# Performance work log

Hardware: AMD Instinct MI355X
Metric: run time of the kernel (lower is better)

## Reference

```python
import jax, jax.numpy as jnp
import numpy as np


def silu(x):
    return x * jax.nn.sigmoid(x)


def conv1x1(x, w, s, b, act):
    # x: [B,Ci,H,W], w: [Co,Ci]; BN folded into per-channel scale s / bias b
    y = jnp.einsum('oi,bihw->bohw', w, x) * s[None, :, None, None] + b[None, :, None, None]
    return silu(y) if act else y


def dwconv3x3(x, w, s, b):
    # depthwise 3x3, groups=C, padding SAME (autopad=1); w: [C,1,3,3]
    y = jax.lax.conv_general_dilated(
        x, w, window_strides=(1, 1), padding=[(1, 1), (1, 1)],
        dimension_numbers=('NCHW', 'OIHW', 'NCHW'),
        feature_group_count=x.shape[1])
    return y * s[None, :, None, None] + b[None, :, None, None]


def attention(x, qkv_w, qkv_s, qkv_b, pe_w, pe_s, pe_b, proj_w, proj_s, proj_b,
              num_heads=4, key_dim=32, head_dim=64):
    B, C, H, W = x.shape
    N = H * W
    scale = key_dim ** -0.5
    qkv = conv1x1(x, qkv_w, qkv_s, qkv_b, act=False)          # [B, C+2*nh*kd, H, W]
    qkv = qkv.reshape(B, num_heads, key_dim * 2 + head_dim, N)
    q = qkv[:, :, :key_dim]                                    # [B,nh,kd,N]
    k = qkv[:, :, key_dim:2 * key_dim]                         # [B,nh,kd,N]
    v = qkv[:, :, 2 * key_dim:]                                # [B,nh,hd,N]
    attn = jnp.einsum('bhdi,bhdj->bhij', q, k) * scale         # [B,nh,N,N]
    attn = jax.nn.softmax(attn, axis=-1)
    out = jnp.einsum('bhdj,bhij->bhdi', v, attn)               # [B,nh,hd,N]
    out = out.reshape(B, C, H, W) + dwconv3x3(v.reshape(B, C, H, W), pe_w, pe_s, pe_b)
    return conv1x1(out, proj_w, proj_s, proj_b, act=False)


def setup_inputs() -> dict:
    key = jax.random.key(0)
    ks = jax.random.split(key, 32)
    B, C1, H, W = 4, 512, 48, 48
    c = C1 // 2  # 256
    h = c + 2 * 32 * 4  # 512
    d = {'x': jax.random.normal(ks[0], (B, C1, H, W), jnp.float32)}
    def w(i, shape):
        return jax.random.normal(ks[i], shape, jnp.float32) * 0.05
    def s(i, n):
        return jax.random.uniform(ks[i], (n,), jnp.float32, 0.5, 1.5)
    def b(i, n):
        return jax.random.normal(ks[i], (n,), jnp.float32) * 0.05
    d['cv1_w'], d['cv1_s'], d['cv1_b'] = w(1, (2 * c, C1)), s(2, 2 * c), b(3, 2 * c)
    d['qkv_w'], d['qkv_s'], d['qkv_b'] = w(4, (h, c)), s(5, h), b(6, h)
    d['pe_w'], d['pe_s'], d['pe_b'] = w(7, (c, 1, 3, 3)), s(8, c), b(9, c)
    d['proj_w'], d['proj_s'], d['proj_b'] = w(10, (c, c)), s(11, c), b(12, c)
    d['ffn1_w'], d['ffn1_s'], d['ffn1_b'] = w(13, (2 * c, c)), s(14, 2 * c), b(15, 2 * c)
    d['ffn2_w'], d['ffn2_s'], d['ffn2_b'] = w(16, (c, 2 * c)), s(17, c), b(18, c)
    d['cv2_w'], d['cv2_s'], d['cv2_b'] = w(19, (C1, 2 * c)), s(20, C1), b(21, C1)
    return d


def reference(x, cv1_w, cv1_s, cv1_b, qkv_w, qkv_s, qkv_b, pe_w, pe_s, pe_b,
              proj_w, proj_s, proj_b, ffn1_w, ffn1_s, ffn1_b, ffn2_w, ffn2_s, ffn2_b,
              cv2_w, cv2_s, cv2_b):
    c = cv1_w.shape[0] // 2  # hidden channels (256)
    ab = conv1x1(x, cv1_w, cv1_s, cv1_b, act=True)
    a, bb = ab[:, :c], ab[:, c:]
    bb = bb + attention(bb, qkv_w, qkv_s, qkv_b, pe_w, pe_s, pe_b,
                        proj_w, proj_s, proj_b)
    f = conv1x1(bb, ffn1_w, ffn1_s, ffn1_b, act=True)
    bb = bb + conv1x1(f, ffn2_w, ffn2_s, ffn2_b, act=False)
    return conv1x1(jnp.concatenate([a, bb], axis=1), cv2_w, cv2_s, cv2_b, act=True)
```

## Files before the change

### kernel.cpp

```cpp
#include <hip/hip_runtime.h>
#include <math.h>

#define N_SP 2304
#define HW 48

typedef unsigned short u16;
typedef short s8v  __attribute__((ext_vector_type(8)));
typedef short s4v  __attribute__((ext_vector_type(4)));
typedef u16   u16x8 __attribute__((ext_vector_type(8)));
typedef float f32x4 __attribute__((ext_vector_type(4)));
typedef unsigned u32x4 __attribute__((ext_vector_type(4)));

__device__ __forceinline__ short f2bf(float x) {
    unsigned u = __float_as_uint(x);
    u += 0x7FFFu + ((u >> 16) & 1u);
    return (short)(u >> 16);
}
__device__ __forceinline__ float bf2f(u16 u) {
    return __uint_as_float((unsigned)u << 16);
}
__device__ __forceinline__ float fexp2(float x) { return __builtin_amdgcn_exp2f(x); }
__device__ __forceinline__ float frcp(float x)  { return __builtin_amdgcn_rcpf(x); }
__device__ __forceinline__ float fsilu(float v) {
    return v * frcp(1.f + fexp2(-1.4426950408889634f * v));
}
__device__ __forceinline__ unsigned cvtpk(float lo, float hi) {
    unsigned r;
    asm("v_cvt_pk_bf16_f32 %0, %1, %2" : "=v"(r) : "v"(lo), "v"(hi));
    return r;
}
__device__ __forceinline__ void gload16(const void* g, void* l) {
    __builtin_amdgcn_global_load_lds(
        (const __attribute__((address_space(1))) void*)g,
        (__attribute__((address_space(3))) void*)l, 16, 0, 0);
}

__global__ __launch_bounds__(256) void cvt_w(
    const float* __restrict__ s0, const float* __restrict__ s1,
    const float* __restrict__ s2, const float* __restrict__ s3,
    const float* __restrict__ s4, const float* __restrict__ s5,
    u16* __restrict__ d0, u16* __restrict__ d1, u16* __restrict__ d2,
    u16* __restrict__ d3, u16* __restrict__ d4, u16* __restrict__ d5)
{
    int id = blockIdx.x * 256 + threadIdx.x;
    const int c0 = 65536, c1 = c0 + 32768, c2 = c1 + 16384,
              c3 = c2 + 32768, c4 = c3 + 32768, c5 = c4 + 65536;
    if (id >= c5) return;
    const float* s; u16* d; int off;
    if      (id < c0) { s = s0; d = d0; off = id; }
    else if (id < c1) { s = s1; d = d1; off = id - c0; }
    else if (id < c2) { s = s2; d = d2; off = id - c1; }
    else if (id < c3) { s = s3; d = d3; off = id - c2; }
    else if (id < c4) { s = s4; d = d4; off = id - c3; }
    else              { s = s5; d = d5; off = id - c4; }
    float4 v = ((const float4*)s)[off];
    s4v p; p[0] = f2bf(v.x); p[1] = f2bf(v.y); p[2] = f2bf(v.z); p[3] = f2bf(v.w);
    ((s4v*)d)[off] = p;
}

__global__ __launch_bounds__(256) void transpose_x(const float* __restrict__ X,
                                                   u16* __restrict__ XT)
{
    __shared__ float tile[64][65];
    const int n0 = blockIdx.x * 64, c0 = blockIdx.y * 64, b = blockIdx.z;
    const float* src = X + (long)b * 512 * N_SP;
    u16* dst = XT + (long)b * N_SP * 512;
    const int t = threadIdx.x;
    #pragma unroll
    for (int it = 0; it < 16; ++it) {
        int id = t + 256 * it;
        int cl = id >> 6, nl = id & 63;
        tile[cl][nl] = src[(long)(c0 + cl) * N_SP + n0 + nl];
    }
    __syncthreads();
    #pragma unroll
    for (int it = 0; it < 16; ++it) {
        int id = t + 256 * it;
        int nl = id >> 6, cl = id & 63;
        dst[(long)(n0 + nl) * 512 + c0 + cl] = f2bf(tile[cl][nl]);
    }
}

template <int BN_, int OMODE>
__global__ __launch_bounds__(256) void mfma_gemm(
    const u16* __restrict__ A1, const u16* __restrict__ A2, int K1,
    int sA1, int sA2, int K,
    const u16* __restrict__ W,
    const float* __restrict__ S, const float* __restrict__ Bi,
    const u16* __restrict__ Res, int sR,
    void* __restrict__ OutP, int sO, int Mtot,
    int act)
{
    constexpr int NFN = BN_ / 32;
    __shared__ u16 Al[2][128][64];
    __shared__ u16 Bl[2][BN_][64];
    const int t  = threadIdx.x;
    const int n0 = blockIdx.x * 128;
    const int o0 = blockIdx.y * BN_;
    const int lane = t & 63, w = t >> 6;
    const int wn = (w & 1) * 64, wo = (w >> 1) * (BN_ / 2);
    const int li = lane & 15, g = lane >> 4;

    const int b_blk = n0 / N_SP;
    const int n_in0 = n0 - b_blk * N_SP;

    f32x4 acc[4][NFN];
    #pragma unroll
    for (int fm = 0; fm < 4; ++fm)
        #pragma unroll
        for (int fn = 0; fn < NFN; ++fn) acc[fm][fn] = f32x4{0.f, 0.f, 0.f, 0.f};

    auto issue = [&](int buf, int k0) {
        #pragma unroll
        for (int q = 0; q < 4; ++q) {
            int c = t + q * 256;
            int row = c >> 3;
            int col = ((c & 7) ^ (row & 7)) * 8;
            int kk = k0 + col;
            const u16* ga = (kk < K1) ? (A1 + (long)(n0 + row) * sA1 + kk)
                                      : (A2 + (long)(n0 + row) * sA2 + (kk - K1));
            gload16(ga, (u16*)Al[buf] + (q * 256 + w * 64) * 8);
        }
        #pragma unroll
        for (int q = 0; q < NFN; ++q) {
            int c = t + q * 256;
            int row = c >> 3;
            int col = ((c & 7) ^ (row & 7)) * 8;
            gload16(W + (long)(o0 + row) * K + k0 + col,
                    (u16*)Bl[buf] + (q * 256 + w * 64) * 8);
        }
    };

    issue(0, 0);
    asm volatile("s_waitcnt vmcnt(0)" ::: "memory");
    __builtin_amdgcn_s_barrier();

    int cur = 0;
    const int NK = K >> 6;
    for (int ks = 0; ks < NK; ++ks) {
        if (ks + 1 < NK) issue(cur ^ 1, (ks + 1) << 6);
        #pragma unroll
        for (int k2 = 0; k2 < 2; ++k2) {
            s8v af[4], bfv[NFN];
            #pragma unroll
            for (int fm = 0; fm < 4; ++fm) {
                int row = wn + fm * 16 + li;
                af[fm] = *(const s8v*)&Al[cur][row][((g + 4 * k2) ^ (li & 7)) * 8];
            }
            #pragma unroll
            for (int fn = 0; fn < NFN; ++fn) {
                int row = wo + fn * 16 + li;
                bfv[fn] = *(const s8v*)&Bl[cur][row][((g + 4 * k2) ^ (li & 7)) * 8];
            }
            #pragma unroll
            for (int fm = 0; fm < 4; ++fm)
                #pragma unroll
                for (int fn = 0; fn < NFN; ++fn)
                    acc[fm][fn] = __builtin_amdgcn_mfma_f32_16x16x32_bf16(
                        af[fm], bfv[fn], acc[fm][fn], 0, 0, 0);
        }
        asm volatile("s_waitcnt vmcnt(0)" ::: "memory");
        __builtin_amdgcn_s_barrier();
        cur ^= 1;
    }

    #pragma unroll
    for (int fn = 0; fn < NFN; ++fn) {
        const int o = o0 + wo + fn * 16 + li;
        const float sc2 = S[o], bi = Bi[o];
        #pragma unroll
        for (int fm = 0; fm < 4; ++fm) {
            const int nb  = n0 + wn + fm * 16 + 4 * g;
            const int nib = n_in0 + wn + fm * 16 + 4 * g;
            float y[4];
            #pragma unroll
            for (int r = 0; r < 4; ++r) {
                float v = acc[fm][fn][r] * sc2 + bi;
                if (act) v = fsilu(v);
                y[r] = v;
            }
            if (Res) {
                #pragma unroll
                for (int r = 0; r < 4; ++r)
                    y[r] += bf2f(Res[(long)(nb + r) * sR + o]);
            }
            if (OMODE == 0) {
                u16* O = (u16*)OutP;
                #pragma unroll
                for (int r = 0; r < 4; ++r)
                    O[(long)(nb + r) * sO + o] = (u16)f2bf(y[r]);
            } else if (OMODE == 1) {
                u16* O = (u16*)OutP + (long)b_blk * Mtot * N_SP + (long)o * N_SP + nib;
                s4v pk;
                #pragma unroll
                for (int r = 0; r < 4; ++r) pk[r] = f2bf(y[r]);
                *(s4v*)O = pk;
            } else {
                float* O = (float*)OutP + (long)b_blk * Mtot * N_SP + (long)o * N_SP + nib;
                *(float4*)O = make_float4(y[0], y[1], y[2], y[3]);
            }
        }
    }
}

__global__ __launch_bounds__(256) void attn_mfma(const u16* __restrict__ qkv,
    u16* __restrict__ Opart, float* __restrict__ mpart, float* __restrict__ lpart)
{
    const int N = N_SP;
    __shared__ u16 Klds[64][40];
    __shared__ u16 Vlds[64][72];

    const int i0 = blockIdx.x * 128;
    const int bh = blockIdx.y;
    const int z  = blockIdx.z;
    const int b = bh >> 2, h = bh & 3;
    const int t = threadIdx.x;
    const int w = t >> 6;
    const int lane = t & 63;
    const int li = lane & 15;
    const int g  = lane >> 4;
    const float qscale = 0.17677669529663687f * 1.4426950408889634f;

    const u16* qp = qkv + ((long)b * 512 + (long)h * 128) * N;
    const u16* kp = qp + 32L * N;
    const u16* vp = qp + 64L * N;

    const int ia = i0 + w * 16 + li;
    const int ib = ia + 64;

    s8v qf[2];
    #pragma unroll
    for (int r = 0; r < 8; ++r) {
        qf[0][r] = f2bf(bf2f(qp[(long)(8 * g + r) * N + ia]) * qscale);
        qf[1][r] = f2bf(bf2f(qp[(long)(8 * g + r) * N + ib]) * qscale);
    }

    f32x4 oacc[2][4];
    #pragma unroll
    for (int q = 0; q < 2; ++q)
        #pragma unroll
        for (int dt = 0; dt < 4; ++dt) oacc[q][dt] = f32x4{0.f, 0.f, 0.f, 0.f};
    float m_run[2] = {-1e30f, -1e30f}, l_run[2] = {0.f, 0.f};

    const int kj  = lane;
    const int kd0 = w * 8;
    const int vd  = t >> 2;
    const int vjb = (t & 3) * 16;

    const int jbase = z * 576;
    u16x8 kr, vr0, vr1;
    {
        const u16* kpp = kp + jbase + kj;
        #pragma unroll
        for (int u = 0; u < 8; ++u) kr[u] = kpp[(long)(kd0 + u) * N];
        vr0 = *(const u16x8*)(vp + (long)vd * N + jbase + vjb);
        vr1 = *(const u16x8*)(vp + (long)vd * N + jbase + vjb + 8);
    }

    for (int j0 = jbase; j0 < jbase + 576; j0 += 64) {
        __syncthreads();
        *(u16x8*)&Klds[kj][kd0]     = kr;
        *(u16x8*)&Vlds[vd][vjb]     = vr0;
        *(u16x8*)&Vlds[vd][vjb + 8] = vr1;
        if (j0 + 64 < jbase + 576) {
            const u16* kpp = kp + (j0 + 64) + kj;
            #pragma unroll
            for (int u = 0; u < 8; ++u) kr[u] = kpp[(long)(kd0 + u) * N];
            vr0 = *(const u16x8*)(vp + (long)vd * N + (j0 + 64) + vjb);
            vr1 = *(const u16x8*)(vp + (long)vd * N + (j0 + 64) + vjb + 8);
        }
        __syncthreads();

        f32x4 sacc[2][4];
        #pragma unroll
        for (int js = 0; js < 4; ++js) {
            s8v kf = *(const s8v*)&Klds[js * 16 + li][8 * g];
            f32x4 zz = f32x4{0.f, 0.f, 0.f, 0.f};
            sacc[0][js] = __builtin_amdgcn_mfma_f32_16x16x32_bf16(kf, qf[0], zz, 0, 0, 0);
            sacc[1][js] = __builtin_amdgcn_mfma_f32_16x16x32_bf16(kf, qf[1], zz, 0, 0, 0);
        }

        #pragma unroll
        for (int q = 0; q < 2; ++q) {
            float tm = -1e30f;
            #pragma unroll
            for (int js = 0; js < 4; ++js)
                #pragma unroll
                for (int r = 0; r < 4; ++r) tm = fmaxf(tm, sacc[q][js][r]);
            tm = fmaxf(tm, __shfl_xor(tm, 16, 64));
            tm = fmaxf(tm, __shfl_xor(tm, 32, 64));
            if (__any(tm > m_run[q] + 8.f)) {
                float mnew = fmaxf(m_run[q], tm);
                float scl  = fexp2(m_run[q] - mnew);
                l_run[q] *= scl;
                #pragma unroll
                for (int dt = 0; dt < 4; ++dt) oacc[q][dt] *= scl;
                m_run[q] = mnew;
            }
            float ts = 0.f;
            #pragma unroll
            for (int js = 0; js < 4; ++js)
                #pragma unroll
                for (int r = 0; r < 4; ++r) {
                    float p = fexp2(sacc[q][js][r] - m_run[q]);
                    sacc[q][js][r] = p;
                    ts += p;
                }
            ts += __shfl_xor(ts, 16, 64);
            ts += __shfl_xor(ts, 32, 64);
            l_run[q] += ts;
        }

        #pragma unroll
        for (int ks = 0; ks < 2; ++ks) {
            s8v pf[2];
            #pragma unroll
            for (int q = 0; q < 2; ++q) {
                u32x4 pw;
                pw[0] = cvtpk(sacc[q][2 * ks][0],     sacc[q][2 * ks][1]);
                pw[1] = cvtpk(sacc[q][2 * ks][2],     sacc[q][2 * ks][3]);
                pw[2] = cvtpk(sacc[q][2 * ks + 1][0], sacc[q][2 * ks + 1][1]);
                pw[3] = cvtpk(sacc[q][2 * ks + 1][2], sacc[q][2 * ks + 1][3]);
                pf[q] = __builtin_bit_cast(s8v, pw);
            }
            #pragma unroll
            for (int dt = 0; dt < 4; ++dt) {
                int d = dt * 16 + li;
                s4v lo = *(const s4v*)&Vlds[d][32 * ks + 4 * g];
                s4v hi = *(const s4v*)&Vlds[d][32 * ks + 16 + 4 * g];
                s8v vf = __builtin_shufflevector(lo, hi, 0, 1, 2, 3, 4, 5, 6, 7);
                oacc[0][dt] = __builtin_amdgcn_mfma_f32_16x16x32_bf16(vf, pf[0], oacc[0][dt], 0, 0, 0);
                oacc[1][dt] = __builtin_amdgcn_mfma_f32_16x16x32_bf16(vf, pf[1], oacc[1][dt], 0, 0, 0);
            }
        }
    }

    const long cb = (long)(z * 16 + bh);
    #pragma unroll
    for (int q = 0; q < 2; ++q) {
        const int i = q ? ib : ia;
        #pragma unroll
        for (int dt = 0; dt < 4; ++dt)
            #pragma unroll
            for (int r = 0; r < 4; ++r)
                Opart[(cb * 64 + dt * 16 + 4 * g + r) * N + i] = (u16)f2bf(oacc[q][dt][r]);
        if (g == 0) {
            mpart[cb * N + i] = m_run[q];
            lpart[cb * N + i] = l_run[q];
        }
    }
}

__global__ __launch_bounds__(256) void attn_combine(
    const u16* __restrict__ Opart, const float* __restrict__ mpart,
    const float* __restrict__ lpart, const u16* __restrict__ qkv,
    const float* __restrict__ pw, const float* __restrict__ ps,
    const float* __restrict__ pb, u16* __restrict__ attnT)
{
    const int N = N_SP;
    const int i0 = blockIdx.x * 64;
    const int bh = blockIdx.y;
    const int b = bh >> 2, h = bh & 3;
    const int t = threadIdx.x;
    const int il = t & 63, dq = t >> 6;
    const int d0 = dq * 16;
    const int i = i0 + il;

    float mm[4], ll[4];
    #pragma unroll
    for (int c = 0; c < 4; ++c) {
        mm[c] = mpart[((long)(c * 16 + bh)) * N + i];
        ll[c] = lpart[((long)(c * 16 + bh)) * N + i];
    }
    float ms = fmaxf(fmaxf(mm[0], mm[1]), fmaxf(mm[2], mm[3]));
    float wc[4], lsum = 0.f;
    #pragma unroll
    for (int c = 0; c < 4; ++c) {
        wc[c] = fexp2(mm[c] - ms);
        lsum += wc[c] * ll[c];
    }
    float inv = frcp(lsum);

    const int y = i / HW, x = i - (i / HW) * HW;
    const int y0ok = (y > 0), y1ok = (y < HW - 1);
    const int x0ok = (x > 0), x1ok = (x < HW - 1);
    const u16* vbase = qkv + ((long)b * 512 + (long)h * 128 + 64) * N;

    u16 ob[16];
    #pragma unroll
    for (int dd = 0; dd < 16; ++dd) {
        const int d = d0 + dd;
        const int cg = h * 64 + d;
        float o = 0.f;
        #pragma unroll
        for (int c = 0; c < 4; ++c)
            o += wc[c] * bf2f(Opart[((long)(c * 16 + bh) * 64 + d) * N + i]);
        o *= inv;
        const u16* src = vbase + (long)d * N;
        const float* w9 = pw + cg * 9;
        float s = 0.f;
        #pragma unroll
        for (int dy = -1; dy <= 1; ++dy) {
            if ((dy < 0 && !y0ok) || (dy > 0 && !y1ok)) continue;
            const u16* row = src + (y + dy) * HW;
            if (x0ok) s += w9[(dy + 1) * 3 + 0] * bf2f(row[x - 1]);
            s += w9[(dy + 1) * 3 + 1] * bf2f(row[x]);
            if (x1ok) s += w9[(dy + 1) * 3 + 2] * bf2f(row[x + 1]);
        }
        o += s * ps[cg] + pb[cg];
        ob[dd] = (u16)f2bf(o);
    }
    u16* dst = attnT + ((long)b * N + i) * 256 + h * 64 + d0;
    *(u16x8*)dst       = *(u16x8*)&ob[0];
    *(u16x8*)(dst + 8) = *(u16x8*)&ob[8];
}

extern "C" void kernel_launch(void* const* d_in, const int* in_sizes, int n_in,
                              void* d_out, int out_size, void* d_ws, size_t ws_size,
                              hipStream_t stream)
{
    const long N = N_SP;
    const float* x      = (const float*)d_in[0];
    const float* cv1_w  = (const float*)d_in[1];
    const float* cv1_s  = (const float*)d_in[2];
    const float* cv1_b  = (const float*)d_in[3];
    const float* qkv_w  = (const float*)d_in[4];
    const float* qkv_s  = (const float*)d_in[5];
    const float* qkv_b  = (const float*)d_in[6];
    const float* pe_w   = (const float*)d_in[7];
    const float* pe_s   = (const float*)d_in[8];
    const float* pe_b   = (const float*)d_in[9];
    const float* proj_w = (const float*)d_in[10];
    const float* proj_s = (const float*)d_in[11];
    const float* proj_b = (const float*)d_in[12];
    const float* ffn1_w = (const float*)d_in[13];
    const float* ffn1_s = (const float*)d_in[14];
    const float* ffn1_b = (const float*)d_in[15];
    const float* ffn2_w = (const float*)d_in[16];
    const float* ffn2_s = (const float*)d_in[17];
    const float* ffn2_b = (const float*)d_in[18];
    const float* cv2_w  = (const float*)d_in[19];
    const float* cv2_s  = (const float*)d_in[20];
    const float* cv2_b  = (const float*)d_in[21];
    float* out = (float*)d_out;

    u16* ws = (u16*)d_ws;
    u16* xT      = ws;
    u16* abT     = xT      + 4L * N * 512;
    u16* qkvb    = abT     + 4L * N * 512;
    u16* attnT   = qkvb    + 4L * N * 512;
    u16* bb2T    = attnT   + 4L * N * 256;
    u16* fT      = bb2T    + 4L * N * 256;
    u16* bb3T    = fT      + 4L * N * 512;
    u16* w_cv1   = bb3T    + 4L * N * 256;
    u16* w_qkv   = w_cv1   + 512L * 512;
    u16* w_proj  = w_qkv   + 512L * 256;
    u16* w_ffn1  = w_proj  + 256L * 256;
    u16* w_ffn2  = w_ffn1  + 512L * 256;
    u16* w_cv2   = w_ffn2  + 256L * 512;
    u16* Opart   = w_cv2   + 512L * 512;
    float* mpart = (float*)(Opart + 4L * 16 * 64 * N);
    float* lpart = mpart + 4L * 16 * N;

    dim3 blk(256);
    const int BIGK = 1 << 28;

    cvt_w<<<960, blk, 0, stream>>>(cv1_w, qkv_w, proj_w, ffn1_w, ffn2_w, cv2_w,
                                   w_cv1, w_qkv, w_proj, w_ffn1, w_ffn2, w_cv2);
    transpose_x<<<dim3(36, 8, 4), blk, 0, stream>>>(x, xT);

    mfma_gemm<64, 0><<<dim3(72, 8), blk, 0, stream>>>(
        xT, nullptr, BIGK, 512, 0, 512, w_cv1, cv1_s, cv1_b,
        nullptr, 0, abT, 512, 512, 1);

    mfma_gemm<64, 1><<<dim3(72, 8), blk, 0, stream>>>(
        abT + 256, nullptr, BIGK, 512, 0, 256, w_qkv, qkv_s, qkv_b,
        nullptr, 0, qkvb, 0, 512, 0);

    attn_mfma<<<dim3(18, 16, 4), blk, 0, stream>>>(qkvb, Opart, mpart, lpart);

    attn_combine<<<dim3(36, 16), blk, 0, stream>>>(
        Opart, mpart, lpart, qkvb, pe_w, pe_s, pe_b, attnT);

    mfma_gemm<32, 0><<<dim3(72, 8), blk, 0, stream>>>(
        attnT, nullptr, BIGK, 256, 0, 256, w_proj, proj_s, proj_b,
        abT + 256, 512, bb2T, 256, 256, 0);

    mfma_gemm<64, 0><<<dim3(72, 8), blk, 0, stream>>>(
        bb2T, nullptr, BIGK, 256, 0, 256, w_ffn1, ffn1_s, ffn1_b,
        nullptr, 0, fT, 512, 512, 1);

    mfma_gemm<32, 0><<<dim3(72, 8), blk, 0, stream>>>(
        fT, nullptr, BIGK, 512, 0, 512, w_ffn2, ffn2_s, ffn2_b,
        bb2T, 256, bb3T, 256, 256, 0);

    mfma_gemm<64, 2><<<dim3(72, 8), blk, 0, stream>>>(
        abT, bb3T, 256, 512, 256, 512, w_cv2, cv2_s, cv2_b,
        nullptr, 0, out, 0, 512, 1);
}
```

Baseline: 147.6 us.

## Shrink GEMM tiles to 64x64 with triple-buffered loads and double-buffer attention K/V

The 1x1-conv GEMMs now use a fixed 64x64 tile and a three-stage LDS ring with partial vmcnt waits, keeping two prefetches in flight. The launch grid doubles so more blocks run on the CUs. The attention kernel double-buffers its K/V LDS tiles so the next tile's stores overlap with the current MFMA work, which removes one barrier per iteration. Smaller tiles reduce per-block data reuse and raise the total global and LDS traffic.

```diff
diff --git a/kernel.cpp b/kernel.cpp
--- a/kernel.cpp
+++ b/kernel.cpp
@@ -33,6 +33,10 @@
     __builtin_amdgcn_global_load_lds(
         (const __attribute__((address_space(1))) void*)g,
         (__attribute__((address_space(3))) void*)l, 16, 0, 0);
+}
+__device__ __forceinline__ void bar_lgkm() {
+    asm volatile("s_waitcnt lgkmcnt(0)" ::: "memory");
+    __builtin_amdgcn_s_barrier();
 }
 
 __global__ __launch_bounds__(256) void cvt_w(
@@ -81,7 +85,7 @@
     }
 }
 
-template <int BN_, int OMODE>
+template <int OMODE>
 __global__ __launch_bounds__(256) void mfma_gemm(
     const u16* __restrict__ A1, const u16* __restrict__ A2, int K1,
     int sA1, int sA2, int K,
@@ -91,28 +95,27 @@
     void* __restrict__ OutP, int sO, int Mtot,
     int act)
 {
-    constexpr int NFN = BN_ / 32;
-    __shared__ u16 Al[2][128][64];
-    __shared__ u16 Bl[2][BN_][64];
+    __shared__ u16 Al[3][64][64];
+    __shared__ u16 Bl[3][64][64];
     const int t  = threadIdx.x;
-    const int n0 = blockIdx.x * 128;
-    const int o0 = blockIdx.y * BN_;
+    const int n0 = blockIdx.x * 64;
+    const int o0 = blockIdx.y * 64;
     const int lane = t & 63, w = t >> 6;
-    const int wn = (w & 1) * 64, wo = (w >> 1) * (BN_ / 2);
+    const int wn = (w & 1) * 32, wo = (w >> 1) * 32;
     const int li = lane & 15, g = lane >> 4;
 
     const int b_blk = n0 / N_SP;
     const int n_in0 = n0 - b_blk * N_SP;
 
-    f32x4 acc[4][NFN];
-    #pragma unroll
-    for (int fm = 0; fm < 4; ++fm)
-        #pragma unroll
-        for (int fn = 0; fn < NFN; ++fn) acc[fm][fn] = f32x4{0.f, 0.f, 0.f, 0.f};
+    f32x4 acc[2][2];
+    #pragma unroll
+    for (int fm = 0; fm < 2; ++fm)
+        #pragma unroll
+        for (int fn = 0; fn < 2; ++fn) acc[fm][fn] = f32x4{0.f, 0.f, 0.f, 0.f};
 
     auto issue = [&](int buf, int k0) {
         #pragma unroll
-        for (int q = 0; q < 4; ++q) {
+        for (int q = 0; q < 2; ++q) {
             int c = t + q * 256;
             int row = c >> 3;
             int col = ((c & 7) ^ (row & 7)) * 8;
@@ -120,56 +123,49 @@
             const u16* ga = (kk < K1) ? (A1 + (long)(n0 + row) * sA1 + kk)
                                       : (A2 + (long)(n0 + row) * sA2 + (kk - K1));
             gload16(ga, (u16*)Al[buf] + (q * 256 + w * 64) * 8);
-        }
-        #pragma unroll
-        for (int q = 0; q < NFN; ++q) {
-            int c = t + q * 256;
-            int row = c >> 3;
-            int col = ((c & 7) ^ (row & 7)) * 8;
             gload16(W + (long)(o0 + row) * K + k0 + col,
                     (u16*)Bl[buf] + (q * 256 + w * 64) * 8);
         }
     };
 
+    const int NK = K >> 6;
     issue(0, 0);
-    asm volatile("s_waitcnt vmcnt(0)" ::: "memory");
-    __builtin_amdgcn_s_barrier();
-
-    int cur = 0;
-    const int NK = K >> 6;
+    if (NK > 1) issue(1, 64);
+
     for (int ks = 0; ks < NK; ++ks) {
-        if (ks + 1 < NK) issue(cur ^ 1, (ks + 1) << 6);
+        if (ks + 1 < NK) asm volatile("s_waitcnt vmcnt(4)" ::: "memory");
+        else             asm volatile("s_waitcnt vmcnt(0)" ::: "memory");
+        __builtin_amdgcn_s_barrier();
+        if (ks + 2 < NK) issue((ks + 2) % 3, (ks + 2) << 6);
+        const int cur = ks % 3;
         #pragma unroll
         for (int k2 = 0; k2 < 2; ++k2) {
-            s8v af[4], bfv[NFN];
-            #pragma unroll
-            for (int fm = 0; fm < 4; ++fm) {
+            s8v af[2], bfv[2];
+            #pragma unroll
+            for (int fm = 0; fm < 2; ++fm) {
                 int row = wn + fm * 16 + li;
                 af[fm] = *(const s8v*)&Al[cur][row][((g + 4 * k2) ^ (li & 7)) * 8];
             }
             #pragma unroll
-            for (int fn = 0; fn < NFN; ++fn) {
+            for (int fn = 0; fn < 2; ++fn) {
                 int row = wo + fn * 16 + li;
                 bfv[fn] = *(const s8v*)&Bl[cur][row][((g + 4 * k2) ^ (li & 7)) * 8];
             }
             #pragma unroll
-            for (int fm = 0; fm < 4; ++fm)
-                #pragma unroll
-                for (int fn = 0; fn < NFN; ++fn)
+            for (int fm = 0; fm < 2; ++fm)
+                #pragma unroll
+                for (int fn = 0; fn < 2; ++fn)
                     acc[fm][fn] = __builtin_amdgcn_mfma_f32_16x16x32_bf16(
                         af[fm], bfv[fn], acc[fm][fn], 0, 0, 0);
         }
-        asm volatile("s_waitcnt vmcnt(0)" ::: "memory");
-        __builtin_amdgcn_s_barrier();
-        cur ^= 1;
-    }
-
-    #pragma unroll
-    for (int fn = 0; fn < NFN; ++fn) {
+    }
+
+    #pragma unroll
+    for (int fn = 0; fn < 2; ++fn) {
         const int o = o0 + wo + fn * 16 + li;
         const float sc2 = S[o], bi = Bi[o];
         #pragma unroll
-        for (int fm = 0; fm < 4; ++fm) {
+        for (int fm = 0; fm < 2; ++fm) {
             const int nb  = n0 + wn + fm * 16 + 4 * g;
             const int nib = n_in0 + wn + fm * 16 + 4 * g;
             float y[4];
@@ -207,8 +203,8 @@
     u16* __restrict__ Opart, float* __restrict__ mpart, float* __restrict__ lpart)
 {
     const int N = N_SP;
-    __shared__ u16 Klds[64][40];
-    __shared__ u16 Vlds[64][72];
+    __shared__ u16 Klds[2][64][40];
+    __shared__ u16 Vlds[2][64][72];
 
     const int i0 = blockIdx.x * 128;
     const int bh = blockIdx.y;
@@ -249,32 +245,34 @@
 
     const int jbase = z * 576;
     u16x8 kr, vr0, vr1;
-    {
-        const u16* kpp = kp + jbase + kj;
+    auto ldregs = [&](int j0) {
+        const u16* kpp = kp + j0 + kj;
         #pragma unroll
         for (int u = 0; u < 8; ++u) kr[u] = kpp[(long)(kd0 + u) * N];
-        vr0 = *(const u16x8*)(vp + (long)vd * N + jbase + vjb);
-        vr1 = *(const u16x8*)(vp + (long)vd * N + jbase + vjb + 8);
-    }
-
-    for (int j0 = jbase; j0 < jbase + 576; j0 += 64) {
-        __syncthreads();
-        *(u16x8*)&Klds[kj][kd0]     = kr;
-        *(u16x8*)&Vlds[vd][vjb]     = vr0;
-        *(u16x8*)&Vlds[vd][vjb + 8] = vr1;
-        if (j0 + 64 < jbase + 576) {
-            const u16* kpp = kp + (j0 + 64) + kj;
-            #pragma unroll
-            for (int u = 0; u < 8; ++u) kr[u] = kpp[(long)(kd0 + u) * N];
-            vr0 = *(const u16x8*)(vp + (long)vd * N + (j0 + 64) + vjb);
-            vr1 = *(const u16x8*)(vp + (long)vd * N + (j0 + 64) + vjb + 8);
-        }
-        __syncthreads();
+        vr0 = *(const u16x8*)(vp + (long)vd * N + j0 + vjb);
+        vr1 = *(const u16x8*)(vp + (long)vd * N + j0 + vjb + 8);
+    };
+
+    ldregs(jbase);
+    *(u16x8*)&Klds[0][kj][kd0]     = kr;
+    *(u16x8*)&Vlds[0][vd][vjb]     = vr0;
+    *(u16x8*)&Vlds[0][vd][vjb + 8] = vr1;
+    ldregs(jbase + 64);
+    bar_lgkm();
+
+    int cur = 0;
+    for (int it = 0; it < 9; ++it) {
+        if (it + 1 < 9) {
+            *(u16x8*)&Klds[cur ^ 1][kj][kd0]     = kr;
+            *(u16x8*)&Vlds[cur ^ 1][vd][vjb]     = vr0;
+            *(u16x8*)&Vlds[cur ^ 1][vd][vjb + 8] = vr1;
+            if (it + 2 < 9) ldregs(jbase + (it + 2) * 64);
+        }
 
         f32x4 sacc[2][4];
         #pragma unroll
         for (int js = 0; js < 4; ++js) {
-            s8v kf = *(const s8v*)&Klds[js * 16 + li][8 * g];
+            s8v kf = *(const s8v*)&Klds[cur][js * 16 + li][8 * g];
             f32x4 zz = f32x4{0.f, 0.f, 0.f, 0.f};
             sacc[0][js] = __builtin_amdgcn_mfma_f32_16x16x32_bf16(kf, qf[0], zz, 0, 0, 0);
             sacc[1][js] = __builtin_amdgcn_mfma_f32_16x16x32_bf16(kf, qf[1], zz, 0, 0, 0);
@@ -326,13 +324,16 @@
             #pragma unroll
             for (int dt = 0; dt < 4; ++dt) {
                 int d = dt * 16 + li;
-                s4v lo = *(const s4v*)&Vlds[d][32 * ks + 4 * g];
-                s4v hi = *(const s4v*)&Vlds[d][32 * ks + 16 + 4 * g];
+                s4v lo = *(const s4v*)&Vlds[cur][d][32 * ks + 4 * g];
+                s4v hi = *(const s4v*)&Vlds[cur][d][32 * ks + 16 + 4 * g];
                 s8v vf = __builtin_shufflevector(lo, hi, 0, 1, 2, 3, 4, 5, 6, 7);
                 oacc[0][dt] = __builtin_amdgcn_mfma_f32_16x16x32_bf16(vf, pf[0], oacc[0][dt], 0, 0, 0);
                 oacc[1][dt] = __builtin_amdgcn_mfma_f32_16x16x32_bf16(vf, pf[1], oacc[1][dt], 0, 0, 0);
             }
         }
+
+        if (it + 1 < 9) bar_lgkm();
+        cur ^= 1;
     }
 
     const long cb = (long)(z * 16 + bh);
@@ -469,11 +470,11 @@
                                    w_cv1, w_qkv, w_proj, w_ffn1, w_ffn2, w_cv2);
     transpose_x<<<dim3(36, 8, 4), blk, 0, stream>>>(x, xT);
 
-    mfma_gemm<64, 0><<<dim3(72, 8), blk, 0, stream>>>(
+    mfma_gemm<0><<<dim3(144, 8), blk, 0, stream>>>(
         xT, nullptr, BIGK, 512, 0, 512, w_cv1, cv1_s, cv1_b,
         nullptr, 0, abT, 512, 512, 1);
 
-    mfma_gemm<64, 1><<<dim3(72, 8), blk, 0, stream>>>(
+    mfma_gemm<1><<<dim3(144, 8), blk, 0, stream>>>(
         abT + 256, nullptr, BIGK, 512, 0, 256, w_qkv, qkv_s, qkv_b,
         nullptr, 0, qkvb, 0, 512, 0);
 
@@ -482,19 +483,19 @@
     attn_combine<<<dim3(36, 16), blk, 0, stream>>>(
         Opart, mpart, lpart, qkvb, pe_w, pe_s, pe_b, attnT);
 
-    mfma_gemm<32, 0><<<dim3(72, 8), blk, 0, stream>>>(
+    mfma_gemm<0><<<dim3(144, 4), blk, 0, stream>>>(
         attnT, nullptr, BIGK, 256, 0, 256, w_proj, proj_s, proj_b,
         abT + 256, 512, bb2T, 256, 256, 0);
 
-    mfma_gemm<64, 0><<<dim3(72, 8), blk, 0, stream>>>(
+    mfma_gemm<0><<<dim3(144, 8), blk, 0, stream>>>(
         bb2T, nullptr, BIGK, 256, 0, 256, w_ffn1, ffn1_s, ffn1_b,
         nullptr, 0, fT, 512, 512, 1);
 
-    mfma_gemm<32, 0><<<dim3(72, 8), blk, 0, stream>>>(
+    mfma_gemm<0><<<dim3(144, 4), blk, 0, stream>>>(
         fT, nullptr, BIGK, 512, 0, 512, w_ffn2, ffn2_s, ffn2_b,
         bb2T, 256, bb3T, 256, 256, 0);
 
-    mfma_gemm<64, 2><<<dim3(72, 8), blk, 0, stream>>>(
+    mfma_gemm<2><<<dim3(144, 8), blk, 0, stream>>>(
         abT, bb3T, 256, 512, 256, 512, w_cv2, cv2_s, cv2_b,
         nullptr, 0, out, 0, 512, 1);
 }
```

New measurement: 148.8 us. No clear change (+0.8%).
